# Kernel tuning notes

Measured on AMD Instinct MI355X. Metric: run time of the kernel, lower is better.

The kernel has to match this reference:

```python
import jax, jax.numpy as jnp
import numpy as np

WINDOW_SIZE = 512
NUM_HEADS = 16
HIDDEN = 1024
HEAD_DIM = HIDDEN // NUM_HEADS
SCALING = HEAD_DIM ** (-0.5)


def sliding_window_mask(seq_len, window_size):
    # row i attends to cols j with i - w//2 <= j <= i + w//2 (clipped to bounds)
    i = jnp.arange(seq_len)[:, None]
    j = jnp.arange(seq_len)[None, :]
    half = window_size // 2
    return jnp.abs(i - j) <= half  # [S, S] bool


def setup_inputs() -> dict:
    key = jax.random.key(0)
    k0, k1, k2, k3, k4 = jax.random.split(key, 5)
    B, S = 2, 2048
    hidden_states = jax.random.normal(k0, (B, S, HIDDEN), dtype=jnp.float32)
    scale = 0.02
    Wq = jax.random.normal(k1, (HIDDEN, HIDDEN), dtype=jnp.float32) * scale
    Wk = jax.random.normal(k2, (HIDDEN, HIDDEN), dtype=jnp.float32) * scale
    Wv = jax.random.normal(k3, (HIDDEN, HIDDEN), dtype=jnp.float32) * scale
    Wo = jax.random.normal(k4, (HIDDEN, HIDDEN), dtype=jnp.float32) * scale
    return {"hidden_states": hidden_states, "Wq": Wq, "Wk": Wk, "Wv": Wv, "Wo": Wo}


def reference(hidden_states, Wq, Wk, Wv, Wo):
    B, S, _ = hidden_states.shape
    # nn.Linear(bias=False): y = x @ W.T
    def proj(x, W):
        y = jnp.einsum('bsh,oh->bso', x, W)
        return y.reshape(B, S, NUM_HEADS, HEAD_DIM).transpose(0, 2, 1, 3)  # [B,H,S,D]

    q = proj(hidden_states, Wq)
    k = proj(hidden_states, Wk)
    v = proj(hidden_states, Wv)

    mask = sliding_window_mask(S, WINDOW_SIZE)  # [S,S]
    scores = jnp.einsum('bhsd,bhtd->bhst', q, k) * SCALING  # [B,H,S,S]
    scores = jnp.where(mask[None, None], scores, -jnp.inf)
    attn = jax.nn.softmax(scores, axis=-1)
    out = jnp.einsum('bhst,bhtd->bhsd', attn, v)
    out = out.transpose(0, 2, 1, 3).reshape(B, S, HIDDEN)
    out = jnp.einsum('bsh,oh->bso', out, Wo)
    return out, attn
```

## Files before the change

kernel.cpp:

```cpp
#include <hip/hip_runtime.h>

typedef unsigned short u16;
typedef __attribute__((ext_vector_type(8))) __bf16 bf16x8;
typedef __attribute__((ext_vector_type(4))) float f32x4;

#define DEV __device__ __forceinline__
#define SEQ 2048
#define SWZ(r) ((((r) & 7)) ^ (((r) >> 3) & 7))

DEV void async16(void* lds, const void* gptr) {
  __builtin_amdgcn_global_load_lds(
      (const __attribute__((address_space(1))) unsigned int*)gptr,
      (__attribute__((address_space(3))) unsigned int*)lds, 16, 0, 0);
}

DEV u16 f2bf(float x) {
  unsigned u = __float_as_uint(x);
  return (u16)((u + 0x7fffu + ((u >> 16) & 1u)) >> 16);
}

DEV f32x4 mfma(bf16x8 a, bf16x8 b, f32x4 c) {
  return __builtin_amdgcn_mfma_f32_16x16x32_bf16(a, b, c, 0, 0, 0);
}

__global__ __launch_bounds__(256) void k_cvt_all(
    const float* __restrict__ hs, const float* __restrict__ wq,
    const float* __restrict__ wk, const float* __restrict__ wv,
    const float* __restrict__ wo, u16* __restrict__ X16,
    u16* __restrict__ W16) {
  int b = blockIdx.x;
  const float* src;
  u16* dst;
  int off;
  if (b < 4096) {
    src = hs;
    dst = X16;
    off = b * 1024;
  } else {
    int b2 = b - 4096;
    int w = b2 >> 10;
    src = (w == 0) ? wq : (w == 1) ? wk : (w == 2) ? wv : wo;
    dst = W16 + (size_t)w * 1048576;
    off = (b2 & 1023) * 1024;
  }
  int i = off + threadIdx.x * 4;
  float4 v = *(const float4*)(src + i);
  *(ushort4*)(dst + i) = make_ushort4(f2bf(v.x), f2bf(v.y), f2bf(v.z), f2bf(v.w));
}

DEV void gemm_mainloop(const u16* __restrict__ A, const u16* __restrict__ B,
                       int K, u16* As, u16* Bs, f32x4 (&acc)[4][4], int tid) {
  const int wid = tid >> 6, lane = tid & 63;
  const int wm = wid >> 1, wn = wid & 1;
  const int quad = lane >> 4, l15 = lane & 15;
  const int ci0 = tid, ci1 = tid + 256;
  const int r0 = ci0 >> 2, g0 = (ci0 & 3) ^ (r0 & 3);
  const int r1 = ci1 >> 2, g1 = (ci1 & 3) ^ (r1 & 3);
  u16* ldsA0 = As + wid * 512;
  u16* ldsA1 = As + wid * 512 + 2048;
  u16* ldsB0 = Bs + wid * 512;
  u16* ldsB1 = Bs + wid * 512 + 2048;

  for (int k0 = 0; k0 < K; k0 += 32) {
    __syncthreads();
    async16(ldsA0, A + (size_t)r0 * K + k0 + g0 * 8);
    async16(ldsA1, A + (size_t)r1 * K + k0 + g1 * 8);
    async16(ldsB0, B + (size_t)r0 * K + k0 + g0 * 8);
    async16(ldsB1, B + (size_t)r1 * K + k0 + g1 * 8);
    __syncthreads();
    bf16x8 af[4], bf[4];
#pragma unroll
    for (int mt = 0; mt < 4; ++mt) {
      int row = wm * 64 + mt * 16 + l15;
      af[mt] = *(const bf16x8*)(As + row * 32 + (quad ^ (row & 3)) * 8);
    }
#pragma unroll
    for (int nt = 0; nt < 4; ++nt) {
      int row = wn * 64 + nt * 16 + l15;
      bf[nt] = *(const bf16x8*)(Bs + row * 32 + (quad ^ (row & 3)) * 8);
    }
#pragma unroll
    for (int mt = 0; mt < 4; ++mt)
#pragma unroll
      for (int nt = 0; nt < 4; ++nt)
        acc[mt][nt] = mfma(af[mt], bf[nt], acc[mt][nt]);
  }
}

__global__ __launch_bounds__(256) void k_gemm_qkv(
    const u16* __restrict__ X, const u16* __restrict__ Wq,
    const u16* __restrict__ Wk, const u16* __restrict__ Wv,
    u16* __restrict__ Q16, u16* __restrict__ K16, u16* __restrict__ V16) {
  __shared__ u16 As[128 * 32], Bs[128 * 32];
  const int tid = threadIdx.x;
  const int bm = blockIdx.x, bn = blockIdx.y, z = blockIdx.z;
  const u16* B = (z == 0) ? Wq : (z == 1) ? Wk : Wv;
  u16* dst = (z == 0) ? Q16 : (z == 1) ? K16 : V16;
  const float sc = (z == 0) ? 0.125f : 1.0f;
  f32x4 acc[4][4];
#pragma unroll
  for (int i = 0; i < 4; ++i)
#pragma unroll
    for (int j = 0; j < 4; ++j) acc[i][j] = (f32x4){0.f, 0.f, 0.f, 0.f};
  gemm_mainloop(X + (size_t)bm * 128 * 1024, B + (size_t)bn * 128 * 1024, 1024,
                As, Bs, acc, tid);
  const int wid = tid >> 6, lane = tid & 63;
  const int wm = wid >> 1, wn = wid & 1, quad = lane >> 4, l15 = lane & 15;
#pragma unroll
  for (int mt = 0; mt < 4; ++mt)
#pragma unroll
    for (int nt = 0; nt < 4; ++nt)
#pragma unroll
      for (int r = 0; r < 4; ++r) {
        int row = bm * 128 + wm * 64 + mt * 16 + quad * 4 + r;
        int col = bn * 128 + wn * 64 + nt * 16 + l15;
        int b = row >> 11, s = row & 2047, h = col >> 6, d = col & 63;
        int bh = b * 16 + h;
        dst[((size_t)bh * SEQ + s) * 64 + d] = f2bf(acc[mt][nt][r] * sc);
      }
}

__global__ __launch_bounds__(256) void k_gemm_out(const u16* __restrict__ A,
                                                  const u16* __restrict__ Bw,
                                                  float* __restrict__ out) {
  __shared__ u16 As[64 * 32], Bs[128 * 32];
  const int tid = threadIdx.x;
  const int wid = tid >> 6, lane = tid & 63;
  const int wm = wid >> 1, wn = wid & 1;
  const int quad = lane >> 4, l15 = lane & 15;
  const int rA = tid >> 2, gA = (tid & 3) ^ (rA & 3);
  const int r1 = (tid + 256) >> 2, g1 = ((tid + 256) & 3) ^ (r1 & 3);
  const u16* Ab = A + (size_t)blockIdx.x * 64 * 1024;
  const u16* Bb = Bw + (size_t)blockIdx.y * 128 * 1024;
  f32x4 acc[2][4];
#pragma unroll
  for (int i = 0; i < 2; ++i)
#pragma unroll
    for (int j = 0; j < 4; ++j) acc[i][j] = (f32x4){0.f, 0.f, 0.f, 0.f};

  for (int k0 = 0; k0 < 1024; k0 += 32) {
    __syncthreads();
    async16(As + wid * 512, Ab + (size_t)rA * 1024 + k0 + gA * 8);
    async16(Bs + wid * 512, Bb + (size_t)rA * 1024 + k0 + gA * 8);
    async16(Bs + wid * 512 + 2048, Bb + (size_t)r1 * 1024 + k0 + g1 * 8);
    __syncthreads();
    bf16x8 af[2], bf[4];
#pragma unroll
    for (int mt = 0; mt < 2; ++mt) {
      int row = wm * 32 + mt * 16 + l15;
      af[mt] = *(const bf16x8*)(As + row * 32 + (quad ^ (row & 3)) * 8);
    }
#pragma unroll
    for (int nt = 0; nt < 4; ++nt) {
      int row = wn * 64 + nt * 16 + l15;
      bf[nt] = *(const bf16x8*)(Bs + row * 32 + (quad ^ (row & 3)) * 8);
    }
#pragma unroll
    for (int mt = 0; mt < 2; ++mt)
#pragma unroll
      for (int nt = 0; nt < 4; ++nt)
        acc[mt][nt] = mfma(af[mt], bf[nt], acc[mt][nt]);
  }
#pragma unroll
  for (int mt = 0; mt < 2; ++mt)
#pragma unroll
    for (int nt = 0; nt < 4; ++nt)
#pragma unroll
      for (int r = 0; r < 4; ++r) {
        int row = blockIdx.x * 64 + wm * 32 + mt * 16 + quad * 4 + r;
        int col = blockIdx.y * 128 + wn * 64 + nt * 16 + l15;
        out[(size_t)row * 1024 + col] = acc[mt][nt][r];
      }
}

__global__ __launch_bounds__(256, 2) void k_attn(
    const u16* __restrict__ Q16, const u16* __restrict__ K16,
    const u16* __restrict__ V16, float* __restrict__ attn_out,
    u16* __restrict__ O16) {
  __shared__ union alignas(16) U {
    struct {
      u16 Qt[4096];
      u16 Kt[2][4096];
      u16 Vt[2][4096];
      u16 P[2][64 * 72];
    } s;
    float Pf[64 * 68];
  } sm;
  __shared__ float rowsum[64];

  const int tid = threadIdx.x, wid = tid >> 6, lane = tid & 63;
  const int quad = lane >> 4, l15 = lane & 15;
  const int qbase = blockIdx.x * 64;
  const int bh = blockIdx.y;
  const int b = bh >> 4, h = bh & 15;
  const u16* Qb = Q16 + ((size_t)bh * SEQ + qbase) * 64;
  const u16* Kb = K16 + (size_t)bh * SEQ * 64;
  const u16* Vb = V16 + (size_t)bh * SEQ * 64;
  float* attn_b = attn_out + (size_t)bh * SEQ * SEQ;

  const int r0 = tid >> 3, g0 = (tid & 7) ^ SWZ(r0);
  const int r1 = r0 + 32, g1 = (tid & 7) ^ SWZ(r1);

  const int tlo = qbase >= 256 ? 0 : (256 - qbase) >> 6;
  const int thi_raw = (SEQ - 64 - qbase + 256) >> 6;
  const int thi = thi_raw > 8 ? 8 : thi_raw;

  async16(sm.s.Qt + wid * 512, Qb + r0 * 64 + g0 * 8);
  async16(sm.s.Qt + wid * 512 + 2048, Qb + (size_t)r1 * 64 + g1 * 8);
  {
    int jb = qbase - 256 + tlo * 64;
    u16* Kd = sm.s.Kt[tlo & 1];
    u16* Vd = sm.s.Vt[tlo & 1];
    async16(Kd + wid * 512, Kb + (size_t)(jb + r0) * 64 + g0 * 8);
    async16(Kd + wid * 512 + 2048, Kb + (size_t)(jb + r1) * 64 + g1 * 8);
    async16(Vd + wid * 512, Vb + (size_t)(jb + r0) * 64 + g0 * 8);
    async16(Vd + wid * 512 + 2048, Vb + (size_t)(jb + r1) * 64 + g1 * 8);
  }
  if (tid < 64) rowsum[tid] = 0.f;

  float racc[4][4];
  f32x4 oacc[4];
#pragma unroll
  for (int mt = 0; mt < 4; ++mt) {
    oacc[mt] = (f32x4){0.f, 0.f, 0.f, 0.f};
#pragma unroll
    for (int r = 0; r < 4; ++r) racc[mt][r] = 0.f;
  }
  unsigned stash[9][8];
  bf16x8 bv_prev[2];
  bf16x8 aq[4][2];
  bool aq_loaded = false;
  const int d = wid * 16 + l15;

#pragma unroll
  for (int t = 0; t < 9; ++t) {
    if (t < tlo || t > thi) continue;
    const int jbase = qbase - 256 + t * 64;
    __syncthreads();
    if (t < thi) {
      int jb = jbase + 64;
      u16* Kd = sm.s.Kt[(t + 1) & 1];
      u16* Vd = sm.s.Vt[(t + 1) & 1];
      async16(Kd + wid * 512, Kb + (size_t)(jb + r0) * 64 + g0 * 8);
      async16(Kd + wid * 512 + 2048, Kb + (size_t)(jb + r1) * 64 + g1 * 8);
      async16(Vd + wid * 512, Vb + (size_t)(jb + r0) * 64 + g0 * 8);
      async16(Vd + wid * 512 + 2048, Vb + (size_t)(jb + r1) * 64 + g1 * 8);
    }
    if (!aq_loaded) {
      aq_loaded = true;
#pragma unroll
      for (int mt = 0; mt < 4; ++mt)
#pragma unroll
        for (int ks = 0; ks < 2; ++ks) {
          int row = mt * 16 + l15;
          aq[mt][ks] = *(const bf16x8*)(sm.s.Qt + row * 64 +
                                        (((ks * 4 + quad) ^ SWZ(row)) * 8));
        }
    }
    if (t > tlo) {
      const u16* Pp = sm.s.P[(t + 1) & 1];
#pragma unroll
      for (int mt = 0; mt < 4; ++mt) {
        int row = mt * 16 + l15;
        bf16x8 ap0 = *(const bf16x8*)(Pp + row * 72 + quad * 8);
        bf16x8 ap1 = *(const bf16x8*)(Pp + row * 72 + 32 + quad * 8);
        oacc[mt] = mfma(ap0, bv_prev[0], oacc[mt]);
        oacc[mt] = mfma(ap1, bv_prev[1], oacc[mt]);
      }
    }
    const u16* Kt = sm.s.Kt[t & 1];
    const u16* Vtp = sm.s.Vt[t & 1];
    bf16x8 bq[2];
#pragma unroll
    for (int ks = 0; ks < 2; ++ks) {
      int row = wid * 16 + l15;
      bq[ks] = *(const bf16x8*)(Kt + row * 64 + (((ks * 4 + quad) ^ SWZ(row)) * 8));
    }
#pragma unroll
    for (int ks = 0; ks < 2; ++ks)
#pragma unroll
      for (int jj = 0; jj < 8; ++jj) {
        int j = ks * 32 + quad * 8 + jj;
        int slot = (d >> 3) ^ SWZ(j);
        bv_prev[ks][jj] = *(const __bf16*)(Vtp + j * 64 + slot * 8 + (d & 7));
      }
    u16* Pc = sm.s.P[t & 1];
    const int jcol = jbase + wid * 16 + l15;
#pragma unroll
    for (int mt = 0; mt < 4; ++mt) {
      f32x4 c = (f32x4){0.f, 0.f, 0.f, 0.f};
      c = mfma(aq[mt][0], bq[0], c);
      c = mfma(aq[mt][1], bq[1], c);
      unsigned p0 = 0, p1 = 0;
#pragma unroll
      for (int r = 0; r < 4; ++r) {
        int i_ = qbase + mt * 16 + quad * 4 + r;
        int dlt = i_ - jcol;
        dlt = dlt < 0 ? -dlt : dlt;
        float e = 0.f;
        if (dlt <= 256) e = __expf(c[r]);
        racc[mt][r] += e;
        unsigned eb = f2bf(e);
        Pc[(mt * 16 + quad * 4 + r) * 72 + wid * 16 + l15] = (u16)eb;
        if (r == 0) p0 = eb;
        if (r == 1) p0 |= eb << 16;
        if (r == 2) p1 = eb;
        if (r == 3) p1 |= eb << 16;
      }
      stash[t][mt * 2] = p0;
      stash[t][mt * 2 + 1] = p1;
    }
  }
  __syncthreads();
  {
    const u16* Pp = sm.s.P[thi & 1];
#pragma unroll
    for (int mt = 0; mt < 4; ++mt) {
      int row = mt * 16 + l15;
      bf16x8 ap0 = *(const bf16x8*)(Pp + row * 72 + quad * 8);
      bf16x8 ap1 = *(const bf16x8*)(Pp + row * 72 + 32 + quad * 8);
      oacc[mt] = mfma(ap0, bv_prev[0], oacc[mt]);
      oacc[mt] = mfma(ap1, bv_prev[1], oacc[mt]);
    }
  }

#pragma unroll
  for (int mt = 0; mt < 4; ++mt)
#pragma unroll
    for (int r = 0; r < 4; ++r) {
      float v = racc[mt][r];
      v += __shfl_xor(v, 1, 16);
      v += __shfl_xor(v, 2, 16);
      v += __shfl_xor(v, 4, 16);
      v += __shfl_xor(v, 8, 16);
      racc[mt][r] = v;
    }
  if (l15 == 0) {
#pragma unroll
    for (int mt = 0; mt < 4; ++mt)
#pragma unroll
      for (int r = 0; r < 4; ++r)
        atomicAdd(&rowsum[mt * 16 + quad * 4 + r], racc[mt][r]);
  }
  __syncthreads();
  float linv[4][4];
#pragma unroll
  for (int mt = 0; mt < 4; ++mt)
#pragma unroll
    for (int r = 0; r < 4; ++r)
      linv[mt][r] = 1.0f / rowsum[mt * 16 + quad * 4 + r];

#pragma unroll
  for (int mt = 0; mt < 4; ++mt)
#pragma unroll
    for (int r = 0; r < 4; ++r) {
      int i_ = qbase + mt * 16 + quad * 4 + r;
      O16[((size_t)b * SEQ + i_) * 1024 + h * 64 + d] =
          f2bf(oacc[mt][r] * linv[mt][r]);
    }

  const int wcol = (tid & 15) * 4, wrow = tid >> 4;
#pragma unroll
  for (int t = 0; t < 9; ++t) {
    if (t < tlo || t > thi) continue;
    const int jbase = qbase - 256 + t * 64;
    __syncthreads();
#pragma unroll
    for (int mt = 0; mt < 4; ++mt) {
      unsigned p0 = stash[t][mt * 2], p1 = stash[t][mt * 2 + 1];
      int rb = mt * 16 + quad * 4;
      int cc = wid * 16 + l15;
      sm.Pf[(rb + 0) * 68 + cc] = __uint_as_float(p0 << 16) * linv[mt][0];
      sm.Pf[(rb + 1) * 68 + cc] = __uint_as_float(p0 & 0xffff0000u) * linv[mt][1];
      sm.Pf[(rb + 2) * 68 + cc] = __uint_as_float(p1 << 16) * linv[mt][2];
      sm.Pf[(rb + 3) * 68 + cc] = __uint_as_float(p1 & 0xffff0000u) * linv[mt][3];
    }
    __syncthreads();
#pragma unroll
    for (int k = 0; k < 4; ++k) {
      int row = wrow + k * 16;
      f32x4 v = *(const f32x4*)(sm.Pf + row * 68 + wcol);
      __builtin_nontemporal_store(
          v, (f32x4*)(attn_b + (size_t)(qbase + row) * SEQ + jbase + wcol));
    }
  }
}

extern "C" void kernel_launch(void* const* d_in, const int* in_sizes, int n_in,
                              void* d_out, int out_size, void* d_ws,
                              size_t ws_size, hipStream_t stream) {
  const float* hs = (const float*)d_in[0];
  const float* Wq = (const float*)d_in[1];
  const float* Wk = (const float*)d_in[2];
  const float* Wv = (const float*)d_in[3];
  const float* Wo = (const float*)d_in[4];
  float* out = (float*)d_out;
  float* attn = out + (size_t)4194304;

  u16* X16 = (u16*)d_ws;
  u16* Wq16 = X16 + 4194304;
  u16* Wk16 = Wq16 + 1048576;
  u16* Wv16 = Wk16 + 1048576;
  u16* Wo16 = Wv16 + 1048576;
  u16* Q16 = Wo16 + 1048576;
  u16* K16 = Q16 + 4194304;
  u16* V16 = K16 + 4194304;
  u16* O16 = V16 + 4194304;

  k_cvt_all<<<8192, 256, 0, stream>>>(hs, Wq, Wk, Wv, Wo, X16, Wq16);
  k_gemm_qkv<<<dim3(32, 8, 3), 256, 0, stream>>>(X16, Wq16, Wk16, Wv16, Q16,
                                                 K16, V16);
  k_attn<<<dim3(32, 32), 256, 0, stream>>>(Q16, K16, V16, attn, O16);
  k_gemm_out<<<dim3(64, 8), 256, 0, stream>>>(O16, Wo16, out);
}
```

Before: 577.1 us.

## Store V transposed from projection and use per-wave slabs for attn writeback

The QKV projection now writes V in a transposed [bh, d, seq] layout with packed 4-element stores, so the attention kernel can load V tiles with async copies and read B-operand fragments as single 16-byte vector loads instead of eight scalar bf16 LDS reads. The attention-probability writeback switches from a block-wide shared tile with two __syncthreads per tile to per-wave private slabs, removing block barriers. The cost is that each wave's global stores now cover only 64-byte row segments, which may coalesce less well, and the transposed V stores are strided in global memory.

```diff
diff --git a/kernel.cpp b/kernel.cpp
--- a/kernel.cpp
+++ b/kernel.cpp
@@ -106,18 +106,35 @@
                 As, Bs, acc, tid);
   const int wid = tid >> 6, lane = tid & 63;
   const int wm = wid >> 1, wn = wid & 1, quad = lane >> 4, l15 = lane & 15;
-#pragma unroll
-  for (int mt = 0; mt < 4; ++mt)
-#pragma unroll
-    for (int nt = 0; nt < 4; ++nt)
-#pragma unroll
-      for (int r = 0; r < 4; ++r) {
-        int row = bm * 128 + wm * 64 + mt * 16 + quad * 4 + r;
+  if (z == 2) {
+#pragma unroll
+    for (int mt = 0; mt < 4; ++mt) {
+      int row = bm * 128 + wm * 64 + mt * 16 + quad * 4;
+      int b = row >> 11, s = row & 2047;
+#pragma unroll
+      for (int nt = 0; nt < 4; ++nt) {
         int col = bn * 128 + wn * 64 + nt * 16 + l15;
-        int b = row >> 11, s = row & 2047, h = col >> 6, d = col & 63;
-        int bh = b * 16 + h;
-        dst[((size_t)bh * SEQ + s) * 64 + d] = f2bf(acc[mt][nt][r] * sc);
+        int h = col >> 6, d = col & 63;
+        ushort4 pk =
+            make_ushort4(f2bf(acc[mt][nt][0]), f2bf(acc[mt][nt][1]),
+                         f2bf(acc[mt][nt][2]), f2bf(acc[mt][nt][3]));
+        *(ushort4*)(dst + ((size_t)((b * 16 + h) * 64 + d)) * SEQ + s) = pk;
       }
+    }
+  } else {
+#pragma unroll
+    for (int mt = 0; mt < 4; ++mt)
+#pragma unroll
+      for (int nt = 0; nt < 4; ++nt)
+#pragma unroll
+        for (int r = 0; r < 4; ++r) {
+          int row = bm * 128 + wm * 64 + mt * 16 + quad * 4 + r;
+          int col = bn * 128 + wn * 64 + nt * 16 + l15;
+          int b = row >> 11, s = row & 2047, h = col >> 6, d = col & 63;
+          int bh = b * 16 + h;
+          dst[((size_t)bh * SEQ + s) * 64 + d] = f2bf(acc[mt][nt][r] * sc);
+        }
+  }
 }
 
 __global__ __launch_bounds__(256) void k_gemm_out(const u16* __restrict__ A,
@@ -184,7 +201,7 @@
       u16 Vt[2][4096];
       u16 P[2][64 * 72];
     } s;
-    float Pf[64 * 68];
+    float slab[4 * 64 * 20];
   } sm;
   __shared__ float rowsum[64];
 
@@ -195,7 +212,7 @@
   const int b = bh >> 4, h = bh & 15;
   const u16* Qb = Q16 + ((size_t)bh * SEQ + qbase) * 64;
   const u16* Kb = K16 + (size_t)bh * SEQ * 64;
-  const u16* Vb = V16 + (size_t)bh * SEQ * 64;
+  const u16* VbT = V16 + (size_t)bh * 64 * SEQ;
   float* attn_b = attn_out + (size_t)bh * SEQ * SEQ;
 
   const int r0 = tid >> 3, g0 = (tid & 7) ^ SWZ(r0);
@@ -213,8 +230,8 @@
     u16* Vd = sm.s.Vt[tlo & 1];
     async16(Kd + wid * 512, Kb + (size_t)(jb + r0) * 64 + g0 * 8);
     async16(Kd + wid * 512 + 2048, Kb + (size_t)(jb + r1) * 64 + g1 * 8);
-    async16(Vd + wid * 512, Vb + (size_t)(jb + r0) * 64 + g0 * 8);
-    async16(Vd + wid * 512 + 2048, Vb + (size_t)(jb + r1) * 64 + g1 * 8);
+    async16(Vd + wid * 512, VbT + (size_t)r0 * SEQ + jb + g0 * 8);
+    async16(Vd + wid * 512 + 2048, VbT + (size_t)r1 * SEQ + jb + g1 * 8);
   }
   if (tid < 64) rowsum[tid] = 0.f;
 
@@ -243,8 +260,8 @@
       u16* Vd = sm.s.Vt[(t + 1) & 1];
       async16(Kd + wid * 512, Kb + (size_t)(jb + r0) * 64 + g0 * 8);
       async16(Kd + wid * 512 + 2048, Kb + (size_t)(jb + r1) * 64 + g1 * 8);
-      async16(Vd + wid * 512, Vb + (size_t)(jb + r0) * 64 + g0 * 8);
-      async16(Vd + wid * 512 + 2048, Vb + (size_t)(jb + r1) * 64 + g1 * 8);
+      async16(Vd + wid * 512, VbT + (size_t)r0 * SEQ + jb + g0 * 8);
+      async16(Vd + wid * 512 + 2048, VbT + (size_t)r1 * SEQ + jb + g1 * 8);
     }
     if (!aq_loaded) {
       aq_loaded = true;
@@ -278,12 +295,8 @@
     }
 #pragma unroll
     for (int ks = 0; ks < 2; ++ks)
-#pragma unroll
-      for (int jj = 0; jj < 8; ++jj) {
-        int j = ks * 32 + quad * 8 + jj;
-        int slot = (d >> 3) ^ SWZ(j);
-        bv_prev[ks][jj] = *(const __bf16*)(Vtp + j * 64 + slot * 8 + (d & 7));
-      }
+      bv_prev[ks] =
+          *(const bf16x8*)(Vtp + d * 64 + (((ks * 4 + quad) ^ SWZ(d)) * 8));
     u16* Pc = sm.s.P[t & 1];
     const int jcol = jbase + wid * 16 + l15;
 #pragma unroll
@@ -359,29 +372,28 @@
           f2bf(oacc[mt][r] * linv[mt][r]);
     }
 
-  const int wcol = (tid & 15) * 4, wrow = tid >> 4;
+  float* slab = sm.slab + wid * 1280;
+  const int srow = lane >> 2, scg = lane & 3;
 #pragma unroll
   for (int t = 0; t < 9; ++t) {
     if (t < tlo || t > thi) continue;
     const int jbase = qbase - 256 + t * 64;
-    __syncthreads();
 #pragma unroll
     for (int mt = 0; mt < 4; ++mt) {
       unsigned p0 = stash[t][mt * 2], p1 = stash[t][mt * 2 + 1];
       int rb = mt * 16 + quad * 4;
-      int cc = wid * 16 + l15;
-      sm.Pf[(rb + 0) * 68 + cc] = __uint_as_float(p0 << 16) * linv[mt][0];
-      sm.Pf[(rb + 1) * 68 + cc] = __uint_as_float(p0 & 0xffff0000u) * linv[mt][1];
-      sm.Pf[(rb + 2) * 68 + cc] = __uint_as_float(p1 << 16) * linv[mt][2];
-      sm.Pf[(rb + 3) * 68 + cc] = __uint_as_float(p1 & 0xffff0000u) * linv[mt][3];
-    }
-    __syncthreads();
+      slab[(rb + 0) * 20 + l15] = __uint_as_float(p0 << 16) * linv[mt][0];
+      slab[(rb + 1) * 20 + l15] = __uint_as_float(p0 & 0xffff0000u) * linv[mt][1];
+      slab[(rb + 2) * 20 + l15] = __uint_as_float(p1 << 16) * linv[mt][2];
+      slab[(rb + 3) * 20 + l15] = __uint_as_float(p1 & 0xffff0000u) * linv[mt][3];
+    }
 #pragma unroll
     for (int k = 0; k < 4; ++k) {
-      int row = wrow + k * 16;
-      f32x4 v = *(const f32x4*)(sm.Pf + row * 68 + wcol);
+      int row = srow + k * 16;
+      f32x4 v = *(const f32x4*)(slab + row * 20 + scg * 4);
       __builtin_nontemporal_store(
-          v, (f32x4*)(attn_b + (size_t)(qbase + row) * SEQ + jbase + wcol));
+          v, (f32x4*)(attn_b + (size_t)(qbase + row) * SEQ + jbase + wid * 16 +
+                      scg * 4));
     }
   }
 }
```

Result: slower. 606.4 us (+5.1%).

## Triple-buffer K/V tiles with explicit waitcnt and use per-wave attn write slabs

Applied to the files above, without the earlier changes.

K/V staging moves from double to triple buffering. Loads are issued two tiles ahead, and s_waitcnt vmcnt plus a raw s_barrier replace __syncthreads, so global-to-LDS loads overlap more compute. The attention-probability writeback now uses a private LDS slab per wave, which removes the two block-wide barriers per tile during the epilogue. The cost is more LDS per block, which may hurt the occupancy of 2 set in launch_bounds, and the correctness now depends on the hand-written vmcnt accounting.

```diff
diff --git a/kernel.cpp b/kernel.cpp
--- a/kernel.cpp
+++ b/kernel.cpp
@@ -180,11 +180,11 @@
   __shared__ union alignas(16) U {
     struct {
       u16 Qt[4096];
-      u16 Kt[2][4096];
-      u16 Vt[2][4096];
+      u16 Kt[3][4096];
+      u16 Vt[3][4096];
       u16 P[2][64 * 72];
     } s;
-    float Pf[64 * 68];
+    float slab[4 * 64 * 20];
   } sm;
   __shared__ float rowsum[64];
 
@@ -205,17 +205,20 @@
   const int thi_raw = (SEQ - 64 - qbase + 256) >> 6;
   const int thi = thi_raw > 8 ? 8 : thi_raw;
 
-  async16(sm.s.Qt + wid * 512, Qb + r0 * 64 + g0 * 8);
-  async16(sm.s.Qt + wid * 512 + 2048, Qb + (size_t)r1 * 64 + g1 * 8);
-  {
-    int jb = qbase - 256 + tlo * 64;
-    u16* Kd = sm.s.Kt[tlo & 1];
-    u16* Vd = sm.s.Vt[tlo & 1];
+  auto stage = [&](int t) {
+    int jb = qbase - 256 + t * 64;
+    u16* Kd = sm.s.Kt[t % 3];
+    u16* Vd = sm.s.Vt[t % 3];
     async16(Kd + wid * 512, Kb + (size_t)(jb + r0) * 64 + g0 * 8);
     async16(Kd + wid * 512 + 2048, Kb + (size_t)(jb + r1) * 64 + g1 * 8);
     async16(Vd + wid * 512, Vb + (size_t)(jb + r0) * 64 + g0 * 8);
     async16(Vd + wid * 512 + 2048, Vb + (size_t)(jb + r1) * 64 + g1 * 8);
-  }
+  };
+
+  async16(sm.s.Qt + wid * 512, Qb + r0 * 64 + g0 * 8);
+  async16(sm.s.Qt + wid * 512 + 2048, Qb + (size_t)r1 * 64 + g1 * 8);
+  stage(tlo);
+  if (tlo + 1 <= thi) stage(tlo + 1);
   if (tid < 64) rowsum[tid] = 0.f;
 
   float racc[4][4];
@@ -236,16 +239,12 @@
   for (int t = 0; t < 9; ++t) {
     if (t < tlo || t > thi) continue;
     const int jbase = qbase - 256 + t * 64;
-    __syncthreads();
-    if (t < thi) {
-      int jb = jbase + 64;
-      u16* Kd = sm.s.Kt[(t + 1) & 1];
-      u16* Vd = sm.s.Vt[(t + 1) & 1];
-      async16(Kd + wid * 512, Kb + (size_t)(jb + r0) * 64 + g0 * 8);
-      async16(Kd + wid * 512 + 2048, Kb + (size_t)(jb + r1) * 64 + g1 * 8);
-      async16(Vd + wid * 512, Vb + (size_t)(jb + r0) * 64 + g0 * 8);
-      async16(Vd + wid * 512 + 2048, Vb + (size_t)(jb + r1) * 64 + g1 * 8);
-    }
+    if (t + 1 <= thi)
+      asm volatile("s_waitcnt vmcnt(4) lgkmcnt(0)" ::: "memory");
+    else
+      asm volatile("s_waitcnt vmcnt(0) lgkmcnt(0)" ::: "memory");
+    __builtin_amdgcn_s_barrier();
+    if (t + 2 <= thi) stage(t + 2);
     if (!aq_loaded) {
       aq_loaded = true;
 #pragma unroll
@@ -268,8 +267,8 @@
         oacc[mt] = mfma(ap1, bv_prev[1], oacc[mt]);
       }
     }
-    const u16* Kt = sm.s.Kt[t & 1];
-    const u16* Vtp = sm.s.Vt[t & 1];
+    const u16* Kt = sm.s.Kt[t % 3];
+    const u16* Vtp = sm.s.Vt[t % 3];
     bf16x8 bq[2];
 #pragma unroll
     for (int ks = 0; ks < 2; ++ks) {
@@ -359,29 +358,28 @@
           f2bf(oacc[mt][r] * linv[mt][r]);
     }
 
-  const int wcol = (tid & 15) * 4, wrow = tid >> 4;
+  float* slab = sm.slab + wid * 1280;
+  const int srow = lane >> 2, scg = lane & 3;
 #pragma unroll
   for (int t = 0; t < 9; ++t) {
     if (t < tlo || t > thi) continue;
     const int jbase = qbase - 256 + t * 64;
-    __syncthreads();
 #pragma unroll
     for (int mt = 0; mt < 4; ++mt) {
       unsigned p0 = stash[t][mt * 2], p1 = stash[t][mt * 2 + 1];
       int rb = mt * 16 + quad * 4;
-      int cc = wid * 16 + l15;
-      sm.Pf[(rb + 0) * 68 + cc] = __uint_as_float(p0 << 16) * linv[mt][0];
-      sm.Pf[(rb + 1) * 68 + cc] = __uint_as_float(p0 & 0xffff0000u) * linv[mt][1];
-      sm.Pf[(rb + 2) * 68 + cc] = __uint_as_float(p1 << 16) * linv[mt][2];
-      sm.Pf[(rb + 3) * 68 + cc] = __uint_as_float(p1 & 0xffff0000u) * linv[mt][3];
-    }
-    __syncthreads();
+      slab[(rb + 0) * 20 + l15] = __uint_as_float(p0 << 16) * linv[mt][0];
+      slab[(rb + 1) * 20 + l15] = __uint_as_float(p0 & 0xffff0000u) * linv[mt][1];
+      slab[(rb + 2) * 20 + l15] = __uint_as_float(p1 << 16) * linv[mt][2];
+      slab[(rb + 3) * 20 + l15] = __uint_as_float(p1 & 0xffff0000u) * linv[mt][3];
+    }
 #pragma unroll
     for (int k = 0; k < 4; ++k) {
-      int row = wrow + k * 16;
-      f32x4 v = *(const f32x4*)(sm.Pf + row * 68 + wcol);
+      int row = srow + k * 16;
+      f32x4 v = *(const f32x4*)(slab + row * 20 + scg * 4);
       __builtin_nontemporal_store(
-          v, (f32x4*)(attn_b + (size_t)(qbase + row) * SEQ + jbase + wcol));
+          v, (f32x4*)(attn_b + (size_t)(qbase + row) * SEQ + jbase + wid * 16 +
+                      scg * 4));
     }
   }
 }
```

Measured after the change: 597.0 us. 3.5% more time.
